# Kernel tuning notes

Hardware: AMD Instinct MI355X
Metric: run time of the kernel (lower is better)

## Reference

```python
import jax, jax.numpy as jnp
import numpy as np

E = 1024
H = 16
D = E // H
MLP = 4096
EPS = 1e-5


def _layernorm(x, g, b):
    mu = jnp.mean(x, axis=-1, keepdims=True)
    var = jnp.mean(jnp.square(x - mu), axis=-1, keepdims=True)
    return (x - mu) * jax.lax.rsqrt(var + EPS) * g + b


def setup_inputs() -> dict:
    key = jax.random.key(0)
    ks = jax.random.split(key, 10)
    s = lambda fan_in: 1.0 / np.sqrt(fan_in)
    return {
        "x": jax.random.normal(ks[0], (4, 2048, E), dtype=jnp.float32),
        "qkv_w": jax.random.uniform(ks[1], (3 * E, E), jnp.float32, -s(E), s(E)),
        "fc_w": jax.random.uniform(ks[2], (E, E), jnp.float32, -s(E), s(E)),
        "fc_b": jax.random.uniform(ks[3], (E,), jnp.float32, -s(E), s(E)),
        "ln1_g": jnp.ones((E,), jnp.float32),
        "ln1_b": jnp.zeros((E,), jnp.float32),
        "ln2_g": jnp.ones((E,), jnp.float32),
        "ln2_b": jnp.zeros((E,), jnp.float32),
        "w1": jax.random.uniform(ks[4], (MLP, E), jnp.float32, -s(E), s(E)),
        "b1": jax.random.uniform(ks[5], (MLP,), jnp.float32, -s(E), s(E)),
        "w2": jax.random.uniform(ks[6], (E, MLP), jnp.float32, -s(MLP), s(MLP)),
        "b2": jax.random.uniform(ks[7], (E,), jnp.float32, -s(MLP), s(MLP)),
    }


def reference(x, qkv_w, fc_w, fc_b, ln1_g, ln1_b, ln2_g, ln2_b, w1, b1, w2, b2):
    B, S, _ = x.shape
    scale = D ** (-0.5)
    # --- attention sublayer ---
    h = _layernorm(x, ln1_g, ln1_b)
    qkv = (h @ qkv_w.T).reshape(B, S, 3, H, D)
    q, k, v = jnp.moveaxis(qkv, 2, 0)            # each [B, S, H, D]
    q = q.transpose(0, 2, 1, 3)                  # [B, H, S, D]
    k = k.transpose(0, 2, 1, 3)
    v = v.transpose(0, 2, 1, 3)
    scores = jnp.einsum("bhqd,bhkd->bhqk", q, k) * scale
    attn = jax.nn.softmax(scores, axis=-1)
    out = jnp.einsum("bhqk,bhkd->bhqd", attn, v)
    out = out.transpose(0, 2, 1, 3).reshape(B, S, E)
    x = x + (out @ fc_w.T + fc_b)
    # --- MLP sublayer ---
    h = _layernorm(x, ln2_g, ln2_b)
    h = jax.nn.gelu(h @ w1.T + b1, approximate=False)
    x = x + (h @ w2.T + b2)
    return x
```

## Files before the change

kernel.cpp:

```cpp
#include <hip/hip_runtime.h>
#include <cstdint>
#include <cmath>

#define EDIM 1024
#define SEQ 2048
#define BATCH 4
#define NHEAD 16
#define HDIM 64
#define MLPD 4096
#define ROWS 8192

typedef unsigned short u16;
typedef __attribute__((ext_vector_type(8))) short short8;
typedef __attribute__((ext_vector_type(4))) float floatx4;

#define AS1 __attribute__((address_space(1)))
#define AS3 __attribute__((address_space(3)))

#define Q_SCALE 0.18033688011112042f

__device__ __forceinline__ void async16(const void* g, void* l) {
  __builtin_amdgcn_global_load_lds((AS1 void*)g, (AS3 void*)l, 16, 0, 0);
}

__device__ __forceinline__ u16 f2bf(float f) {
  union { float f; unsigned int u; } v; v.f = f;
  unsigned int u = v.u;
  u += 0x7fffu + ((u >> 16) & 1u);
  return (u16)(u >> 16);
}

__device__ __forceinline__ unsigned int u32of(float f) {
  union { float f; unsigned int u; } v; v.f = f; return v.u;
}

__device__ __forceinline__ unsigned int pack_trunc(float a, float b) {
  return __builtin_amdgcn_perm(u32of(b), u32of(a), 0x07060302u);
}

__device__ __forceinline__ float exp2_fast(float x) {
  return __builtin_amdgcn_exp2f(x);
}

__device__ __forceinline__ float gelu_f(float x) {
  const float y = 0.7978845608028654f * (x + 0.044715f * x * x * x);
  const float e = exp2_fast(y * 2.885390081777927f);
  const float t = 1.0f - 2.0f * __builtin_amdgcn_rcpf(1.0f + e);
  return 0.5f * x * (1.0f + t);
}

__global__ __launch_bounds__(256) void cvt_all(const float* __restrict__ a, u16* __restrict__ oa, int na,
                                               const float* __restrict__ b, u16* __restrict__ ob, int nb,
                                               const float* __restrict__ c, u16* __restrict__ oc, int nc,
                                               const float* __restrict__ d, u16* __restrict__ od) {
  int i = (blockIdx.x * 256 + threadIdx.x) * 4;
  const float* src;
  u16* dst;
  if (i < na) { src = a; dst = oa; }
  else if ((i -= na) < nb) { src = b; dst = ob; }
  else if ((i -= nb) < nc) { src = c; dst = oc; }
  else { i -= nc; src = d; dst = od; }
  const float4 v = *(const float4*)(src + i);
  dst[i + 0] = f2bf(v.x); dst[i + 1] = f2bf(v.y);
  dst[i + 2] = f2bf(v.z); dst[i + 3] = f2bf(v.w);
}

__global__ __launch_bounds__(256) void ln_bf16(const float* __restrict__ x,
                                               const float* __restrict__ g,
                                               const float* __restrict__ bta,
                                               u16* __restrict__ outp) {
  const int row = blockIdx.x;
  const int tid = threadIdx.x;
  const float4 v = *(const float4*)(x + (size_t)row * EDIM + tid * 4);
  float s = v.x + v.y + v.z + v.w;
  float ss = v.x * v.x + v.y * v.y + v.z * v.z + v.w * v.w;
#pragma unroll
  for (int o = 1; o < 64; o <<= 1) {
    s += __shfl_xor(s, o);
    ss += __shfl_xor(ss, o);
  }
  __shared__ float red[8];
  const int wave = tid >> 6, lane = tid & 63;
  if (lane == 0) { red[wave] = s; red[4 + wave] = ss; }
  __syncthreads();
  s = red[0] + red[1] + red[2] + red[3];
  ss = red[4] + red[5] + red[6] + red[7];
  const float mu = s * (1.0f / 1024.0f);
  const float var = ss * (1.0f / 1024.0f) - mu * mu;
  const float inv = rsqrtf(var + 1e-5f);
  const float4 gv = *(const float4*)(g + tid * 4);
  const float4 bv = *(const float4*)(bta + tid * 4);
  u16* od = outp + (size_t)row * EDIM + tid * 4;
  od[0] = f2bf((v.x - mu) * inv * gv.x + bv.x);
  od[1] = f2bf((v.y - mu) * inv * gv.y + bv.y);
  od[2] = f2bf((v.z - mu) * inv * gv.z + bv.z);
  od[3] = f2bf((v.w - mu) * inv * gv.w + bv.w);
}

template <int EPI, int BM = 256>
__global__ __launch_bounds__(512) void gemm_bt(const u16* __restrict__ A,
                                               const u16* __restrict__ Bw,
                                               void* __restrict__ Cout,
                                               const float* __restrict__ bias,
                                               const float* __restrict__ res,
                                               int M, int N, int K) {
  constexpr int IB = BM / 64;
  constexpr int WROWS = BM / 4;
  __shared__ __align__(16) u16 As[BM * 64];
  __shared__ __align__(16) u16 Bs[128 * 64];
  const int tid = threadIdx.x;
  const int lane = tid & 63;
  const int wave = tid >> 6;
  const int quad = lane >> 4;
  const int cl = lane & 15;
  const int row0 = blockIdx.y * BM;
  const int col0 = blockIdx.x * 128;
  const int wm = wave >> 1;
  const int wn = wave & 1;

  floatx4 acc[IB][4];
#pragma unroll
  for (int i = 0; i < IB; ++i)
#pragma unroll
    for (int j = 0; j < 4; ++j) acc[i][j] = (floatx4){0.f, 0.f, 0.f, 0.f};

  const int trow = tid >> 3;
  const int gc = (tid & 7) ^ (trow & 7);
  const u16* Ath = A + (size_t)(row0 + trow) * K + gc * 8;
  const u16* Bth = Bw + (size_t)(col0 + trow) * K + gc * 8;
  u16* lA = As + tid * 8;
  u16* lB = Bs + tid * 8;
  const size_t pstride = (size_t)64 * K;

  for (int k0 = 0; k0 < K; k0 += 64) {
    __syncthreads();
#pragma unroll
    for (int p = 0; p < BM / 64; ++p)
      async16(Ath + p * pstride + k0, lA + p * 4096);
#pragma unroll
    for (int p = 0; p < 2; ++p)
      async16(Bth + p * pstride + k0, lB + p * 4096);
    __syncthreads();
#pragma unroll
    for (int s = 0; s < 2; ++s) {
      const int ko = ((s * 4 + quad) ^ (cl & 7)) * 8;
      short8 af[IB], bfr[4];
#pragma unroll
      for (int i = 0; i < IB; ++i)
        af[i] = *(const short8*)(As + (wm * WROWS + i * 16 + cl) * 64 + ko);
#pragma unroll
      for (int j = 0; j < 4; ++j)
        bfr[j] = *(const short8*)(Bs + (wn * 64 + j * 16 + cl) * 64 + ko);
#pragma unroll
      for (int i = 0; i < IB; ++i)
#pragma unroll
        for (int j = 0; j < 4; ++j)
          acc[i][j] = __builtin_amdgcn_mfma_f32_16x16x32_bf16(af[i], bfr[j], acc[i][j], 0, 0, 0);
    }
  }

  const float qscale = (EPI == 5 && col0 < 1024) ? Q_SCALE : 1.0f;
#pragma unroll
  for (int i = 0; i < IB; ++i) {
#pragma unroll
    for (int r = 0; r < 4; ++r) {
      const int row = row0 + wm * WROWS + i * 16 + quad * 4 + r;
#pragma unroll
      for (int j = 0; j < 4; ++j) {
        const int col = col0 + wn * 64 + j * 16 + cl;
        const size_t idx = (size_t)row * N + col;
        float v = acc[i][j][r];
        if (EPI == 0) {
          ((float*)Cout)[idx] = v;
        } else if (EPI == 1 || EPI == 3) {
          ((float*)Cout)[idx] = v + bias[col] + res[idx];
        } else if (EPI == 2) {
          ((u16*)Cout)[idx] = f2bf(gelu_f(v + bias[col]));
        } else if (EPI == 4) {
          ((u16*)Cout)[idx] = f2bf(v);
        } else if (EPI == 5) {
          ((u16*)Cout)[idx] = f2bf(v * qscale);
        }
      }
    }
  }
}

__global__ __launch_bounds__(256) void vtrans(const u16* __restrict__ qkv,
                                              u16* __restrict__ vt) {
  __shared__ unsigned int T[64 * 65];
  const int tid = threadIdx.x;
  const int bh = blockIdx.y;
  const int b = bh >> 4;
  const int h = bh & 15;
  const int s0 = blockIdx.x * 64;
#pragma unroll
  for (int pp = 0; pp < 2; ++pp) {
    const int g = pp * 256 + tid;
    const int r = g >> 3;
    const int d0 = (g & 7) * 8;
    const u16* src = qkv + (size_t)(b * SEQ + s0 + r) * 3072 + 2048 + h * 64 + d0;
    short8 v = *(const short8*)src;
#pragma unroll
    for (int i = 0; i < 8; ++i) T[(d0 + i) * 65 + r] = (u16)v[i];
  }
  __syncthreads();
#pragma unroll
  for (int pp = 0; pp < 2; ++pp) {
    const int g = pp * 256 + tid;
    const int d = g >> 3;
    const int sc = (g & 7) * 8;
    short8 v;
#pragma unroll
    for (int i = 0; i < 8; ++i) v[i] = (short)(u16)T[d * 65 + sc + i];
    *(short8*)(vt + ((size_t)bh * 64 + d) * SEQ + s0 + sc) = v;
  }
}

__global__ __launch_bounds__(256, 4) void attn3(const u16* __restrict__ qkv,
                                                const u16* __restrict__ vt,
                                                u16* __restrict__ outp) {
  __shared__ __align__(16) u16 smem[8192 + 8192 + 4 * 32 * 72];
  u16* Ks = smem;
  u16* Vs = smem + 8192;
  const int tid = threadIdx.x;
  const int lane = tid & 63;
  const int wave = tid >> 6;
  const int quad = lane >> 4;
  const int cl = lane & 15;

  const int f = blockIdx.y * 16 + blockIdx.x;
  const int xcd = f & 7;
  const int u = f >> 3;
  const int qi = u & 15;
  const int bh = xcd * 8 + (u >> 4);
  const int b = bh >> 4;
  const int h = bh & 15;
  const int q0 = qi * 128;
  u16* Pw = smem + 16384 + wave * (32 * 72);

  const u16* qbase = qkv + (size_t)(b * SEQ) * 3072 + h * 64;
  const u16* kbase = qbase + 1024;
  const u16* vbase = vt + (size_t)bh * 64 * SEQ;

#pragma unroll
  for (int p = 0; p < 4; ++p) {
    const int g = (wave * 4 + p) * 64 + lane;
    const int r = g >> 3;
    const int c = (g & 7) ^ (r & 7);
    async16(qbase + (size_t)(q0 + r) * 3072 + c * 8, smem + g * 8);
  }
  __syncthreads();
  short8 qf[2][2];
#pragma unroll
  for (int ng = 0; ng < 2; ++ng)
#pragma unroll
    for (int kc = 0; kc < 2; ++kc) {
      const int row = wave * 32 + ng * 16 + cl;
      qf[ng][kc] = *(const short8*)(smem + row * 64 + (((kc * 4 + quad) ^ (cl & 7)) * 8));
    }

  floatx4 O[4][2];
  float lrun[2] = {0.f, 0.f};
#pragma unroll
  for (int mg = 0; mg < 4; ++mg)
#pragma unroll
    for (int ng = 0; ng < 2; ++ng) O[mg][ng] = (floatx4){0.f, 0.f, 0.f, 0.f};

  for (int kt = 0; kt < SEQ / 128; ++kt) {
    const int k0 = kt * 128;
    __syncthreads();
    const u16* kb = kbase + (size_t)k0 * 3072;
#pragma unroll
    for (int p = 0; p < 2; ++p) {
      const int g = wave * 128 + p * 64 + lane;
      const int rk = g >> 3;
      const int ck = (g & 7) ^ (rk & 7);
      async16(kb + (size_t)rk * 3072 + ck * 8, Ks + g * 8);
      const int rv = g >> 4;
      const int cv = (g & 15) ^ (rv & 15);
      async16(vbase + (size_t)rv * SEQ + k0 + cv * 8, Vs + g * 8);
    }
    __syncthreads();

#pragma unroll
    for (int s = 0; s < 2; ++s) {
      floatx4 Sc[4][2];
#pragma unroll
      for (int mg = 0; mg < 4; ++mg)
#pragma unroll
        for (int ng = 0; ng < 2; ++ng) Sc[mg][ng] = (floatx4){0.f, 0.f, 0.f, 0.f};
#pragma unroll
      for (int kc = 0; kc < 2; ++kc) {
        short8 kf[4];
#pragma unroll
        for (int mg = 0; mg < 4; ++mg) {
          const int row = s * 64 + mg * 16 + cl;
          kf[mg] = *(const short8*)(Ks + row * 64 + (((kc * 4 + quad) ^ (cl & 7)) * 8));
        }
#pragma unroll
        for (int mg = 0; mg < 4; ++mg)
#pragma unroll
          for (int ng = 0; ng < 2; ++ng)
            Sc[mg][ng] = __builtin_amdgcn_mfma_f32_16x16x32_bf16(kf[mg], qf[ng][kc], Sc[mg][ng], 0, 0, 0);
      }

#pragma unroll
      for (int ng = 0; ng < 2; ++ng) {
        float rs = 0.f;
#pragma unroll
        for (int mg = 0; mg < 4; ++mg)
#pragma unroll
          for (int r = 0; r < 4; ++r) {
            const float pv = exp2_fast(Sc[mg][ng][r]);
            Sc[mg][ng][r] = pv;
            rs += pv;
          }
        rs += __shfl_xor(rs, 16);
        rs += __shfl_xor(rs, 32);
        lrun[ng] += rs;
      }

#pragma unroll
      for (int mg = 0; mg < 4; ++mg)
#pragma unroll
        for (int ng = 0; ng < 2; ++ng) {
          const unsigned int lo = pack_trunc(Sc[mg][ng][0], Sc[mg][ng][1]);
          const unsigned int hi = pack_trunc(Sc[mg][ng][2], Sc[mg][ng][3]);
          *(uint2*)(Pw + (ng * 16 + cl) * 72 + mg * 16 + quad * 4) = make_uint2(lo, hi);
        }

#pragma unroll
      for (int kc = 0; kc < 2; ++kc) {
        short8 pf[2], vf[4];
#pragma unroll
        for (int ng = 0; ng < 2; ++ng)
          pf[ng] = *(const short8*)(Pw + (ng * 16 + cl) * 72 + kc * 32 + quad * 8);
#pragma unroll
        for (int mg = 0; mg < 4; ++mg) {
          const int row = mg * 16 + cl;
          vf[mg] = *(const short8*)(Vs + row * 128 + (((s * 8 + kc * 4 + quad) ^ (cl & 15)) * 8));
        }
#pragma unroll
        for (int mg = 0; mg < 4; ++mg)
#pragma unroll
          for (int ng = 0; ng < 2; ++ng)
            O[mg][ng] = __builtin_amdgcn_mfma_f32_16x16x32_bf16(vf[mg], pf[ng], O[mg][ng], 0, 0, 0);
      }
    }
  }

#pragma unroll
  for (int ng = 0; ng < 2; ++ng) {
    const float inv = 1.0f / lrun[ng];
    const int qrow = q0 + wave * 32 + ng * 16 + cl;
    u16* od = outp + (size_t)(b * SEQ + qrow) * EDIM + h * 64;
#pragma unroll
    for (int mg = 0; mg < 4; ++mg) {
      const unsigned int lo = (unsigned int)f2bf(O[mg][ng][0] * inv) |
                              ((unsigned int)f2bf(O[mg][ng][1] * inv) << 16);
      const unsigned int hi = (unsigned int)f2bf(O[mg][ng][2] * inv) |
                              ((unsigned int)f2bf(O[mg][ng][3] * inv) << 16);
      *(uint2*)(od + mg * 16 + quad * 4) = make_uint2(lo, hi);
    }
  }
}

extern "C" void kernel_launch(void* const* d_in, const int* in_sizes, int n_in,
                              void* d_out, int out_size, void* d_ws, size_t ws_size,
                              hipStream_t stream) {
  const float* x    = (const float*)d_in[0];
  const float* qkvw = (const float*)d_in[1];
  const float* fcw  = (const float*)d_in[2];
  const float* fcb  = (const float*)d_in[3];
  const float* ln1g = (const float*)d_in[4];
  const float* ln1b = (const float*)d_in[5];
  const float* ln2g = (const float*)d_in[6];
  const float* ln2b = (const float*)d_in[7];
  const float* w1   = (const float*)d_in[8];
  const float* b1   = (const float*)d_in[9];
  const float* w2   = (const float*)d_in[10];
  const float* b2   = (const float*)d_in[11];

  char* ws = (char*)d_ws;
  size_t off = 0;
  u16* wqkv = (u16*)(ws + off); off += (size_t)3 * EDIM * EDIM * 2;
  u16* wfc  = (u16*)(ws + off); off += (size_t)EDIM * EDIM * 2;
  u16* w1b  = (u16*)(ws + off); off += (size_t)MLPD * EDIM * 2;
  u16* w2b  = (u16*)(ws + off); off += (size_t)EDIM * MLPD * 2;
  u16* hbuf = (u16*)(ws + off); off += (size_t)ROWS * EDIM * 2;
  u16* aout = (u16*)(ws + off); off += (size_t)ROWS * EDIM * 2;
  float* x2 = (float*)(ws + off); off += (size_t)ROWS * EDIM * 4;
  u16* qkvb = (u16*)(ws + off); off += (size_t)ROWS * 3 * EDIM * 2;
  u16* vtb  = (u16*)(ws + off); off += (size_t)ROWS * EDIM * 2;
  u16* hmlp = qkvb;

  cvt_all<<<12288, 256, 0, stream>>>(qkvw, wqkv, 3 * EDIM * EDIM,
                                     fcw, wfc, EDIM * EDIM,
                                     w1, w1b, MLPD * EDIM,
                                     w2, w2b);

  ln_bf16<<<ROWS, 256, 0, stream>>>(x, ln1g, ln1b, hbuf);
  gemm_bt<5><<<dim3(24, 32), 512, 0, stream>>>(hbuf, wqkv, qkvb, nullptr, nullptr,
                                               ROWS, 3 * EDIM, EDIM);
  vtrans<<<dim3(SEQ / 64, 64), 256, 0, stream>>>(qkvb, vtb);
  attn3<<<dim3(16, 64), 256, 0, stream>>>(qkvb, vtb, aout);
  gemm_bt<1, 128><<<dim3(8, 64), 512, 0, stream>>>(aout, wfc, x2, fcb, x,
                                                   ROWS, EDIM, EDIM);
  ln_bf16<<<ROWS, 256, 0, stream>>>(x2, ln2g, ln2b, hbuf);
  gemm_bt<2><<<dim3(32, 32), 512, 0, stream>>>(hbuf, w1b, hmlp, b1, nullptr,
                                               ROWS, MLPD, EDIM);
  gemm_bt<3, 128><<<dim3(8, 64), 512, 0, stream>>>(hmlp, w2b, (float*)d_out, b2, x2,
                                                   ROWS, EDIM, MLPD);
}
```

Baseline: 507.9 us.

## Add 256-row tile GEMM with interleaved async prefetch for QKV and MLP

```diff
diff --git a/kernel.cpp b/kernel.cpp
--- a/kernel.cpp
+++ b/kernel.cpp
@@ -186,6 +186,132 @@
   }
 }
 
+template <int EPI, int BN>
+__global__ __launch_bounds__(512, 2) void gemm8(const u16* __restrict__ A,
+                                                const u16* __restrict__ Bw,
+                                                void* __restrict__ Cout,
+                                                const float* __restrict__ bias,
+                                                const float* __restrict__ res,
+                                                int M, int N, int K) {
+  constexpr int BHALF = BN / 128;
+  constexpr int REG = 2 + BHALF;
+  constexpr int NF = BN / 64;
+  constexpr int DBS = REG * 8192;
+  __shared__ __align__(16) u16 lds[2 * REG * 8192];
+
+  const int tid = threadIdx.x;
+  const int lane = tid & 63;
+  const int wave = tid >> 6;
+  const int quad = lane >> 4;
+  const int cl = lane & 15;
+  const int wm = wave >> 2;
+  const int wn = wave & 3;
+  const int row0 = blockIdx.y * 256;
+  const int col0 = blockIdx.x * BN;
+
+  const int trow = tid >> 3;
+  const int gc = (tid & 7) ^ (trow & 7);
+  const size_t aoff = (size_t)(row0 + trow) * K + gc * 8;
+  const size_t boff = (size_t)(col0 + trow) * K + gc * 8;
+  const size_t rstride = (size_t)128 * K;
+  const size_t hstride = (size_t)64 * K;
+
+  const int aro = wm * 8192 + cl * 64;
+  const int bro = (BN == 256) ? ((2 + (wn >> 1)) * 8192 + ((wn & 1) * 64 + cl) * 64)
+                              : (2 * 8192 + (wn * 32 + cl) * 64);
+  const int ko0 = ((0 + quad) ^ (cl & 7)) * 8;
+  const int ko1 = ((4 + quad) ^ (cl & 7)) * 8;
+
+  floatx4 acc[8][NF];
+#pragma unroll
+  for (int i = 0; i < 8; ++i)
+#pragma unroll
+    for (int j = 0; j < NF; ++j) acc[i][j] = (floatx4){0.f, 0.f, 0.f, 0.f};
+
+  const int nt = K >> 6;
+
+#pragma unroll
+  for (int r = 0; r < REG; ++r) {
+    const u16* s0 = (r < 2) ? (A + aoff + (size_t)r * rstride)
+                            : (Bw + boff + (size_t)(r - 2) * rstride);
+    async16(s0, lds + r * 8192 + tid * 8);
+    async16(s0 + hstride, lds + r * 8192 + 4096 + tid * 8);
+  }
+  asm volatile("s_waitcnt vmcnt(0)" ::: "memory");
+  __builtin_amdgcn_s_barrier();
+  __builtin_amdgcn_sched_barrier(0);
+
+  short8 bf[NF][2];
+
+  for (int t = 0; t < nt; ++t) {
+    u16* cb = lds + (t & 1) * DBS;
+    u16* nb = lds + ((t + 1) & 1) * DBS;
+    const int kn = (t + 1) * 64;
+    const bool more = (t + 1 < nt);
+#pragma unroll
+    for (int q = 0; q < 4; ++q) {
+      short8 a00 = *(const short8*)(cb + aro + (2 * q + 0) * 1024 + ko0);
+      short8 a01 = *(const short8*)(cb + aro + (2 * q + 0) * 1024 + ko1);
+      short8 a10 = *(const short8*)(cb + aro + (2 * q + 1) * 1024 + ko0);
+      short8 a11 = *(const short8*)(cb + aro + (2 * q + 1) * 1024 + ko1);
+      if (q == 0) {
+#pragma unroll
+        for (int n = 0; n < NF; ++n) {
+          bf[n][0] = *(const short8*)(cb + bro + n * 1024 + ko0);
+          bf[n][1] = *(const short8*)(cb + bro + n * 1024 + ko1);
+        }
+      }
+      if (q < REG && more) {
+        const u16* s0 = (q < 2) ? (A + aoff + (size_t)q * rstride + kn)
+                                : (Bw + boff + (size_t)(q - 2) * rstride + kn);
+        async16(s0, nb + q * 8192 + tid * 8);
+        async16(s0 + hstride, nb + q * 8192 + 4096 + tid * 8);
+      }
+      __builtin_amdgcn_s_barrier();
+      asm volatile("s_waitcnt lgkmcnt(0)" ::: "memory");
+      __builtin_amdgcn_sched_barrier(0);
+      __builtin_amdgcn_s_setprio(1);
+#pragma unroll
+      for (int n = 0; n < NF; ++n) {
+        acc[2 * q + 0][n] = __builtin_amdgcn_mfma_f32_16x16x32_bf16(a00, bf[n][0], acc[2 * q + 0][n], 0, 0, 0);
+        acc[2 * q + 0][n] = __builtin_amdgcn_mfma_f32_16x16x32_bf16(a01, bf[n][1], acc[2 * q + 0][n], 0, 0, 0);
+        acc[2 * q + 1][n] = __builtin_amdgcn_mfma_f32_16x16x32_bf16(a10, bf[n][0], acc[2 * q + 1][n], 0, 0, 0);
+        acc[2 * q + 1][n] = __builtin_amdgcn_mfma_f32_16x16x32_bf16(a11, bf[n][1], acc[2 * q + 1][n], 0, 0, 0);
+      }
+      __builtin_amdgcn_s_setprio(0);
+      if (q == 3) { asm volatile("s_waitcnt vmcnt(0)" ::: "memory"); }
+      __builtin_amdgcn_s_barrier();
+      __builtin_amdgcn_sched_barrier(0);
+    }
+  }
+
+  const float qscale = (EPI == 5 && col0 < 1024) ? Q_SCALE : 1.0f;
+#pragma unroll
+  for (int i = 0; i < 8; ++i) {
+#pragma unroll
+    for (int r = 0; r < 4; ++r) {
+      const int row = row0 + wm * 128 + i * 16 + quad * 4 + r;
+#pragma unroll
+      for (int j = 0; j < NF; ++j) {
+        const int col = col0 + wn * (BN / 4) + j * 16 + cl;
+        const size_t idx = (size_t)row * N + col;
+        float v = acc[i][j][r];
+        if (EPI == 0) {
+          ((float*)Cout)[idx] = v;
+        } else if (EPI == 1 || EPI == 3) {
+          ((float*)Cout)[idx] = v + bias[col] + res[idx];
+        } else if (EPI == 2) {
+          ((u16*)Cout)[idx] = f2bf(gelu_f(v + bias[col]));
+        } else if (EPI == 4) {
+          ((u16*)Cout)[idx] = f2bf(v);
+        } else if (EPI == 5) {
+          ((u16*)Cout)[idx] = f2bf(v * qscale);
+        }
+      }
+    }
+  }
+}
+
 __global__ __launch_bounds__(256) void vtrans(const u16* __restrict__ qkv,
                                               u16* __restrict__ vt) {
   __shared__ unsigned int T[64 * 65];
@@ -401,15 +527,15 @@
                                      w2, w2b);
 
   ln_bf16<<<ROWS, 256, 0, stream>>>(x, ln1g, ln1b, hbuf);
-  gemm_bt<5><<<dim3(24, 32), 512, 0, stream>>>(hbuf, wqkv, qkvb, nullptr, nullptr,
-                                               ROWS, 3 * EDIM, EDIM);
+  gemm8<5, 256><<<dim3(12, 32), 512, 0, stream>>>(hbuf, wqkv, qkvb, nullptr, nullptr,
+                                                  ROWS, 3 * EDIM, EDIM);
   vtrans<<<dim3(SEQ / 64, 64), 256, 0, stream>>>(qkvb, vtb);
   attn3<<<dim3(16, 64), 256, 0, stream>>>(qkvb, vtb, aout);
   gemm_bt<1, 128><<<dim3(8, 64), 512, 0, stream>>>(aout, wfc, x2, fcb, x,
                                                    ROWS, EDIM, EDIM);
   ln_bf16<<<ROWS, 256, 0, stream>>>(x2, ln2g, ln2b, hbuf);
-  gemm_bt<2><<<dim3(32, 32), 512, 0, stream>>>(hbuf, w1b, hmlp, b1, nullptr,
-                                               ROWS, MLPD, EDIM);
-  gemm_bt<3, 128><<<dim3(8, 64), 512, 0, stream>>>(hmlp, w2b, (float*)d_out, b2, x2,
-                                                   ROWS, EDIM, MLPD);
-}
+  gemm8<2, 256><<<dim3(16, 32), 512, 0, stream>>>(hbuf, w1b, hmlp, b1, nullptr,
+                                                  ROWS, MLPD, EDIM);
+  gemm8<3, 128><<<dim3(8, 32), 512, 0, stream>>>(hmlp, w2b, (float*)d_out, b2, x2,
+                                                 ROWS, EDIM, MLPD);
+}
```

Measured after the change: 542.5 us. +6.8%, slower.
